# Kernel tuning notes

Measured on AMD Instinct MI355X. Metric: run time of the kernel, lower is better.

The kernel has to match this reference:

```python
import math
import jax, jax.numpy as jnp
import numpy as np

NEG = -1.0e10  # matches LARGE_NUMBER padding in the original
K_SUBSET = 8
N_SAMPLES = 2


def log_conv(aL, aR, K):
    """Log-space convolution of two count distributions, truncated to counts 0..K-1.
    aL, aR: [..., K] log-values; returns c[m] = logsumexp_j aL[j] + aR[m-j]."""
    jj = jnp.arange(K)[:, None]
    mm = jnp.arange(K)[None, :]
    idx = mm - jj  # [K(j), K(m)]
    valid = idx >= 0
    aRg = aR[..., jnp.clip(idx, 0, K - 1)]  # [..., K, K]
    t = aL[..., :, None] + jnp.where(valid, aRg, NEG)
    return jax.nn.logsumexp(t, axis=-2)


def up_pass(theta, k):
    """theta: [B, N] logits (N power of two). Returns list of per-level log-ESP
    tables, levels[l]: [B, N/2^l, k+1]; levels[-1][:,0,j] = log e_j(exp theta)."""
    B, N = theta.shape
    K = k + 1
    leaf = jnp.full((B, N, K), NEG, theta.dtype)
    leaf = leaf.at[..., 0].set(0.0).at[..., 1].set(theta)
    levels = [leaf]
    a = leaf
    while a.shape[1] > 1:
        a = log_conv(a[:, 0::2], a[:, 1::2], K)
        levels.append(a)
    return levels


def down_marginals(levels, theta, k):
    """Exact inclusion marginals P(x_i=1 | sum=k) via tree forward-backward."""
    K = k + 1
    B = theta.shape[0]
    ext = jnp.full((B, 1, K), NEG, theta.dtype).at[..., 0].set(0.0)
    for lvl in range(len(levels) - 2, -1, -1):
        a = levels[lvl]
        aL, aR = a[:, 0::2], a[:, 1::2]
        extL = log_conv(ext, aR, K)  # ESP of everything outside left subtree
        extR = log_conv(ext, aL, K)
        ext = jnp.stack([extL, extR], axis=2).reshape(B, a.shape[1], K)
    logZ = levels[-1][:, 0, k]  # log e_k over all items
    # P(x_i=1) = exp(theta_i) * e_{k-1}(others) / e_k(all)
    return jnp.exp(theta + ext[..., k - 1] - logZ[:, None])


def sample_counts(levels, k, n_samples, key):
    """Top-down exact sampling of k-subsets; returns leaf counts [S, B, N] in {0,1}."""
    K = k + 1
    B = levels[0].shape[0]
    counts = jnp.full((n_samples, B, 1), k, jnp.int32)
    jj = jnp.arange(K)
    for lvl in range(len(levels) - 2, -1, -1):
        a = levels[lvl]
        aL, aR = a[:, 0::2], a[:, 1::2]
        n = aL.shape[1]
        idx = counts[..., None] - jj  # desired right-count, [S,B,n,K]
        valid = idx >= 0
        aRg = jnp.take_along_axis(
            jnp.broadcast_to(aR[None], (n_samples, B, n, K)),
            jnp.clip(idx, 0, k), axis=-1)
        logits = aL[None] + jnp.where(valid, aRg, NEG)
        key, sub = jax.random.split(key)
        g = jax.random.gumbel(sub, logits.shape, logits.dtype)
        cL = jnp.argmax(logits + g, axis=-1).astype(jnp.int32)
        cR = counts - cL
        counts = jnp.stack([cL, cR], axis=-1).reshape(n_samples, B, 2 * n)
    return counts


def setup_inputs() -> dict:
    key = jax.random.key(0)
    scores = jax.random.normal(key, (8192, 32, 8), dtype=jnp.float32)
    return {"scores": scores}


def reference(scores):
    nnodes, choices, ensemble = scores.shape
    k = min(K_SUBSET, choices)
    flat = jnp.transpose(scores, (0, 2, 1)).reshape(nnodes * ensemble, choices)
    N = 2 ** math.ceil(math.log2(choices))
    if N > choices:
        flat = jnp.concatenate(
            [flat, jnp.full((flat.shape[0], N - choices), NEG, flat.dtype)], axis=1)
    levels = up_pass(flat, k)
    marg_flat = down_marginals(levels, flat, k)[:, :choices]  # [B, choices]
    marginals = jnp.transpose(
        marg_flat.reshape(nnodes, ensemble, choices), (0, 2, 1))  # [nnodes, choices, ensemble]
    counts = sample_counts(levels, k, N_SAMPLES, jax.random.key(42))
    counts = counts[:, :, :choices].astype(scores.dtype)
    samples = jnp.transpose(
        counts.reshape(N_SAMPLES, nnodes, ensemble, choices), (0, 1, 3, 2))
    # straight-through: hard samples forward, marginal gradients backward
    samples = jax.lax.stop_gradient(samples - marginals[None]) + marginals[None]
    return samples, marginals
```

## Files before the change

### kernel.cpp

```cpp
#include <hip/hip_runtime.h>
#include <stdint.h>


__host__ __device__ __forceinline__ void tf2x32(uint32_t k0, uint32_t k1,
                                                uint32_t x0, uint32_t x1,
                                                uint32_t& y0, uint32_t& y1) {
  const uint32_t ks[3] = {k0, k1, k0 ^ k1 ^ 0x1BD11BDAu};
  x0 += ks[0]; x1 += ks[1];
  const int R0[4] = {13, 15, 26, 6};
  const int R1[4] = {17, 29, 16, 24};
#pragma unroll
  for (int i = 0; i < 5; ++i) {
    const int* R = (i & 1) ? R1 : R0;
#pragma unroll
    for (int rr = 0; rr < 4; ++rr) {
      x0 += x1;
      x1 = (x1 << R[rr]) | (x1 >> (32 - R[rr]));
      x1 ^= x0;
    }
    x0 += ks[(i + 1) % 3];
    x1 += ks[(i + 2) % 3] + (uint32_t)(i + 1);
  }
  y0 = x0; y1 = x1;
}

struct TFKeys { uint32_t v[10]; };

__device__ __forceinline__ float gumbel_draw(uint32_t sk0, uint32_t sk1,
                                             uint32_t f) {
  uint32_t y0, y1;
  tf2x32(sk0, sk1, 0u, f, y0, y1);
  uint32_t bits = y0 ^ y1;
  uint32_t fb = (bits >> 9) | 0x3f800000u;
  float u = __uint_as_float(fb) - 1.0f;
  const float tiny = 1.17549435e-38f;
  float rr = fmaxf(tiny, u + tiny);
  return -logf(-logf(rr));
}

template<bool FAST> __device__ __forceinline__ float expT(float x) {
  return FAST ? __expf(x) : expf(x);
}
template<bool FAST> __device__ __forceinline__ float logT(float x) {
  return FAST ? __logf(x) : logf(x);
}

template<int SIN, int SOUT, bool FAST, bool LS>
__device__ __forceinline__ void conv_level(const float (&aL)[SIN],
                                           const float (&aR)[SIN],
                                           float (&o)[SOUT]) {
#pragma unroll
  for (int m = 1; m < SOUT; ++m) {
    if (LS && m == SOUT - 1) { o[m] = aL[SIN - 1] + aR[SIN - 1]; continue; }
    const int jlo = (m - (SIN - 1) > 0) ? (m - (SIN - 1)) : 0;
    const int jhi = (m < SIN - 1) ? m : (SIN - 1);
    float t[SIN];
#pragma unroll
    for (int j = 0; j < SIN; ++j)
      if (j >= jlo && j <= jhi) t[j] = aL[j] + aR[m - j];
    float amax = t[jlo];
#pragma unroll
    for (int j = 0; j < SIN; ++j)
      if (j > jlo && j <= jhi) amax = fmaxf(amax, t[j]);
    float s = 0.0f;
#pragma unroll
    for (int j = 0; j < SIN; ++j)
      if (j >= jlo && j <= jhi) s += expT<FAST>(t[j] - amax);
    o[m] = logT<FAST>(s) + amax;
  }
}

template<int SSIB, int MLO, int MHI, bool FAST>
__device__ __forceinline__ void ext_level(const float (&ein)[8],
                                          const float* sib, float (&eo)[8]) {
#pragma unroll
  for (int m = MLO; m <= MHI; ++m) {
    const int jlo = (m - (SSIB - 1) > 0) ? (m - (SSIB - 1)) : 0;
    float t[8];
#pragma unroll
    for (int j = 0; j < 8; ++j)
      if (j >= jlo && j <= m) t[j] = ein[j] + sib[m - j];
    float amax = t[jlo];
#pragma unroll
    for (int j = 0; j < 8; ++j)
      if (j > jlo && j <= m) amax = fmaxf(amax, t[j]);
    float s = 0.0f;
#pragma unroll
    for (int j = 0; j < 8; ++j)
      if (j >= jlo && j <= m) s += expT<FAST>(t[j] - amax);
    eo[m] = logT<FAST>(s) + amax;
  }
}

#define ENT 128

__global__ __launch_bounds__(256, 4) void simple_sampler_kernel(
    const float* __restrict__ scores, float* __restrict__ out,
    int nnodes, TFKeys keys) {
  const int wl = threadIdx.x & 63;
  const int w  = threadIdx.x >> 6;
  const int q = wl & 3;
  const int r = wl >> 2;
  const int p = q & 1;
  const int g = q >> 1;
  const int row = blockIdx.x * 64 + w * 16 + r;
  const int node = row >> 3, e = row & 7;
  const int B = nnodes * 8;

  __shared__ float tab[4 * ENT * 16];
  float* tw = tab + w * (ENT * 16);
#define L(E) tw[(E) * 16 + r]

  float th[8];
  const float* sc = scores + node * 256 + e + (16 * p + 8 * g) * 8;
#pragma unroll
  for (int c = 0; c < 8; ++c) th[c] = sc[c * 8];
#pragma unroll
  for (int c = 0; c < 8; ++c) L(16 * p + 8 * g + c) = th[c];

  float l1r[4], th2r[4];
#pragma unroll
  for (int n1l = 0; n1l < 4; ++n1l) {
    float tL = th[2 * n1l], tR = th[2 * n1l + 1];
    float amax = fmaxf(tR, tL);
    float s = expf(tR - amax) + expf(tL - amax);
    l1r[n1l] = logf(s) + amax;
    th2r[n1l] = tL + tR;
    int n1 = 8 * p + 4 * g + n1l;
    L(32 + n1) = l1r[n1l];
    L(48 + n1) = th2r[n1l];
  }
  float l2r[2][5];
#pragma unroll
  for (int n2l = 0; n2l < 2; ++n2l) {
    float aL[3] = {0.0f, l1r[2 * n2l], th2r[2 * n2l]};
    float aR[3] = {0.0f, l1r[2 * n2l + 1], th2r[2 * n2l + 1]};
    float o5[5];
    conv_level<3, 5, false, true>(aL, aR, o5);
    l2r[n2l][0] = 0.0f;
    int n2 = 4 * p + 2 * g + n2l;
#pragma unroll
    for (int m = 1; m < 5; ++m) { l2r[n2l][m] = o5[m]; L(64 + n2 * 4 + m - 1) = o5[m]; }
  }
  float l3r[9];
  {
    float o9[9];
    conv_level<5, 9, false, true>(l2r[0], l2r[1], o9);
    l3r[0] = 0.0f;
    int n3 = 2 * p + g;
#pragma unroll
    for (int m = 1; m < 9; ++m) { l3r[m] = o9[m]; L(96 + n3 * 8 + m - 1) = o9[m]; }
  }

  __builtin_amdgcn_wave_barrier();

  float l3s[9];
  l3s[0] = 0.0f;
#pragma unroll
  for (int m = 1; m < 9; ++m) l3s[m] = __shfl_xor(l3r[m], 2);

  float A0[9], A1[9];
  {
    float aLp[9], aRp[9];
#pragma unroll
    for (int m = 0; m < 9; ++m) {
      aLp[m] = g ? l3s[m] : l3r[m];
      aRp[m] = g ? l3r[m] : l3s[m];
    }
    float l4o[9];
    conv_level<9, 9, false, false>(aLp, aRp, l4o);
    A0[0] = 0.0f; A1[0] = 0.0f;
#pragma unroll
    for (int m = 1; m < 9; ++m) {
      float own = l4o[m];
      float oth = __shfl_xor(own, 1);
      A0[m] = p ? oth : own;
      A1[m] = p ? own : oth;
    }
  }

  float logZ;
  {
    float tv[9];
#pragma unroll
    for (int j = 0; j < 9; ++j) tv[j] = A0[j] + A1[8 - j];
    float amax = tv[0];
#pragma unroll
    for (int j = 1; j < 9; ++j) amax = fmaxf(amax, tv[j]);
    float s = 0.0f;
#pragma unroll
    for (int j = 0; j < 9; ++j) s += __expf(tv[j] - amax);
    logZ = __logf(s) + amax;
  }

  {
    float e4v[8];
    e4v[0] = 0.0f;
#pragma unroll
    for (int m = 1; m < 8; ++m) e4v[m] = p ? A0[m] : A1[m];
    float* mb = out + 2 * B * 32 + node * 256 + e;
    float e3[8];
    ext_level<9, 0, 7, true>(e4v, l3s, e3);
#pragma unroll
    for (int c2 = 0; c2 < 2; ++c2) {
      float e2v[8];
      ext_level<5, 4, 7, true>(e3, l2r[c2 ^ 1], e2v);
#pragma unroll
      for (int c1i = 0; c1i < 2; ++c1i) {
        const int n1l = 2 * c2 + c1i;
        float sib1[3] = {0.0f, l1r[n1l ^ 1], th2r[n1l ^ 1]};
        float e1m[8];
        ext_level<3, 6, 7, true>(e2v, sib1, e1m);
        const int colL = 16 * p + 8 * g + 2 * n1l;
        {
          float t6 = e1m[6] + th[2 * n1l + 1];
          float t7 = e1m[7];
          float amax = fmaxf(t6, t7);
          float s = __expf(t6 - amax) + __expf(t7 - amax);
          mb[colL * 8] = __expf((th[2 * n1l] + (__logf(s) + amax)) - logZ);
        }
        {
          float t6 = e1m[6] + th[2 * n1l];
          float t7 = e1m[7];
          float amax = fmaxf(t6, t7);
          float s = __expf(t6 - amax) + __expf(t7 - amax);
          mb[(colL + 1) * 8] = __expf((th[2 * n1l + 1] + (__logf(s) + amax)) - logZ);
        }
      }
    }
  }

  const int smp = q & 1;
  const int h = q >> 1;
  const uint32_t t9 = (uint32_t)(smp * B + row) * 9u;
  int c;
  {
    float bv = 0.0f; int bj = 0;
#pragma unroll
    for (int k = 0; k < 5; ++k) {
      const int j = 4 * h + k;
      float gd = gumbel_draw(keys.v[0], keys.v[1], t9 + (uint32_t)j);
      float v = (A0[j] + A1[8 - j]) + gd;
      if (k == 0) { bv = v; bj = j; } else if (v > bv) { bv = v; bj = j; }
    }
    float ov = __shfl_xor(bv, 2);
    int   oj = __shfl_xor(bj, 2);
    float vlo = h ? ov : bv;  int jlo = h ? oj : bj;
    float vhi = h ? bv : ov;  int jhi = h ? bj : oj;
    int rootj = (vhi > vlo) ? jhi : jlo;
    c = h ? (8 - rootj) : rootj;
  }
  int cA, cB;
  {
    int j0 = 0;
    if (c > 0) {
      float b0 = -3.0e38f;
      for (int j = 0; j <= c; ++j) {
        float a = (j == 0) ? 0.0f : L(96 + 16 * h + j - 1);
        float b = (c - j == 0) ? 0.0f : L(96 + 16 * h + 8 + (c - j) - 1);
        float gd = gumbel_draw(keys.v[2], keys.v[3],
                               2u * t9 + (uint32_t)(9 * h + j));
        float v = (a + b) + gd;
        if (v > b0) { b0 = v; j0 = j; }
      }
    }
    cA = j0; cB = c - j0;
  }
  uint32_t pk2 = 0;
  {
    int cc0 = cA, cc1 = cB;
#pragma unroll
    for (int i2 = 0; i2 < 2; ++i2) {
      const int i = 2 * h + i2;
      int ci = i2 ? cc1 : cc0;
      float best = -3.0e38f; int bj2 = 0;
#pragma unroll
      for (int j = 0; j < 5; ++j) {
        float gd = gumbel_draw(keys.v[4], keys.v[5],
                               4u * t9 + (uint32_t)(i * 9 + j));
        int idx = ci - j;
        int cl = min(max(idx, 1), 4);
        float b = L(64 + (2 * i + 1) * 4 + cl - 1);
        float bf = (idx == 0) ? 0.0f : b;
        float a = (j == 0) ? 0.0f : L(64 + (2 * i) * 4 + j - 1);
        float v = (a + bf) + gd;
        if (idx >= 0 && idx <= 4 && v > best) { best = v; bj2 = j; }
      }
      pk2 |= ((uint32_t)bj2 << (8 * i2)) | ((uint32_t)(ci - bj2) << (8 * i2 + 4));
    }
  }
  uint32_t pk3 = 0;
  {
    const uint32_t sk0 = keys.v[6], sk1 = keys.v[7];
    const uint32_t fb0 = 8u * t9;
#pragma unroll
    for (int i2 = 0; i2 < 4; ++i2) {
      const int i = 4 * h + i2;
      int ci = (int)((pk2 >> (4 * i2)) & 15u);
      float aL1 = L(32 + 2 * i), aL2 = L(48 + 2 * i);
      float bR1 = L(32 + 2 * i + 1), bR2 = L(48 + 2 * i + 1);
      uint32_t fb = fb0 + (uint32_t)(i * 9);
      float best = -3.0e38f; int bj3 = 0;
#pragma unroll
      for (int j = 0; j < 3; ++j) {
        float gd = gumbel_draw(sk0, sk1, fb + (uint32_t)j);
        int idx = ci - j;
        float bf = (idx == 1) ? bR1 : ((idx == 2) ? bR2 : 0.0f);
        float af = (j == 0) ? 0.0f : ((j == 1) ? aL1 : aL2);
        float v = (af + bf) + gd;
        if (idx >= 0 && idx <= 2 && v > best) { best = v; bj3 = j; }
      }
      pk3 |= ((uint32_t)bj3 << (8 * i2)) | ((uint32_t)(ci - bj3) << (8 * i2 + 4));
    }
  }
  {
    const uint32_t sk0 = keys.v[8], sk1 = keys.v[9];
    const uint32_t fb0 = 16u * t9;
    float* bs = out + smp * (B * 32) + node * 256 + e;
    uint32_t lst = 0; int m4 = 0;
#pragma unroll
    for (int i2 = 0; i2 < 8; ++i2) {
      int ci = (int)((pk3 >> (4 * i2)) & 15u);
      const int i = 8 * h + i2;
      if (ci == 1) {
        lst |= ((uint32_t)i2) << (4 * m4);
        ++m4;
      } else {
        int bj = ci >> 1;
        bs[16 * i] = (float)bj;
        bs[16 * i + 8] = (float)(ci - bj);
      }
    }
    for (int tt = 0; tt < m4; ++tt) {
      int i2 = (int)((lst >> (4 * tt)) & 15u);
      int i = 8 * h + i2;
      float thL = L(2 * i);
      float thR = L(2 * i + 1);
      uint32_t fb = fb0 + (uint32_t)(i * 9);
      float g0 = gumbel_draw(sk0, sk1, fb);
      float g1 = gumbel_draw(sk0, sk1, fb + 1u);
      int bj = ((thL + g1) > (thR + g0)) ? 1 : 0;
      bs[16 * i] = (float)bj;
      bs[16 * i + 8] = (float)(1 - bj);
    }
  }
#undef L
}

extern "C" void kernel_launch(void* const* d_in, const int* in_sizes, int n_in,
                              void* d_out, int out_size, void* d_ws, size_t ws_size,
                              hipStream_t stream) {
  const float* scores = (const float*)d_in[0];
  float* out = (float*)d_out;
  const int nnodes = in_sizes[0] / (32 * 8);
  const int B = nnodes * 8;

  TFKeys K;
  uint32_t k0 = 0u, k1 = 42u;
  for (int t = 0; t < 5; ++t) {
    uint32_t n0, n1, s0, s1;
    tf2x32(k0, k1, 0u, 0u, n0, n1);
    tf2x32(k0, k1, 0u, 1u, s0, s1);
    K.v[2 * t] = s0; K.v[2 * t + 1] = s1;
    k0 = n0; k1 = n1;
  }

  dim3 grid((unsigned)(B / 64)), block(256);
  hipLaunchKernelGGL(simple_sampler_kernel, grid, block, 0, stream,
                     scores, out, nnodes, K);
}
```

Before: 115.2 us.

## Use one-wave blocks, pad LDS table, and split level-4 convolution across lane pairs

```diff
diff --git a/kernel.cpp b/kernel.cpp
--- a/kernel.cpp
+++ b/kernel.cpp
@@ -94,22 +94,20 @@
 
 #define ENT 128
 
-__global__ __launch_bounds__(256, 4) void simple_sampler_kernel(
+__global__ __launch_bounds__(64, 4) void simple_sampler_kernel(
     const float* __restrict__ scores, float* __restrict__ out,
     int nnodes, TFKeys keys) {
-  const int wl = threadIdx.x & 63;
-  const int w  = threadIdx.x >> 6;
-  const int q = wl & 3;
-  const int r = wl >> 2;
+  const int lane = threadIdx.x;
+  const int q = lane & 3;
+  const int r = lane >> 2;
   const int p = q & 1;
   const int g = q >> 1;
-  const int row = blockIdx.x * 64 + w * 16 + r;
+  const int row = blockIdx.x * 16 + r;
   const int node = row >> 3, e = row & 7;
   const int B = nnodes * 8;
 
-  __shared__ float tab[4 * ENT * 16];
-  float* tw = tab + w * (ENT * 16);
-#define L(E) tw[(E) * 16 + r]
+  __shared__ float tab[ENT * 17];
+#define L(E) tab[(E) * 17 + r]
 
   float th[8];
   const float* sc = scores + node * 256 + e + (16 * p + 8 * g) * 8;
@@ -167,15 +165,40 @@
       aLp[m] = g ? l3s[m] : l3r[m];
       aRp[m] = g ? l3r[m] : l3s[m];
     }
+    float own[4];
+#pragma unroll
+    for (int mi = 0; mi < 4; ++mi) {
+      float t[8];
+#pragma unroll
+      for (int j = 0; j <= 2 * mi + 1; ++j) {
+        float aRv = g ? aRp[2 * mi + 2 - j] : aRp[2 * mi + 1 - j];
+        t[j] = aLp[j] + aRv;
+      }
+      float tlast = aLp[2 * mi + 2] + aRp[0];
+      float amax = t[0];
+#pragma unroll
+      for (int j = 1; j <= 2 * mi + 1; ++j) amax = fmaxf(amax, t[j]);
+      amax = g ? fmaxf(amax, tlast) : amax;
+      float s = 0.0f;
+#pragma unroll
+      for (int j = 0; j <= 2 * mi + 1; ++j) s += expf(t[j] - amax);
+      s += g ? expf(tlast - amax) : 0.0f;
+      own[mi] = logf(s) + amax;
+    }
     float l4o[9];
-    conv_level<9, 9, false, false>(aLp, aRp, l4o);
+#pragma unroll
+    for (int mi = 0; mi < 4; ++mi) {
+      float oth = __shfl_xor(own[mi], 2);
+      l4o[2 * mi + 1] = g ? oth : own[mi];
+      l4o[2 * mi + 2] = g ? own[mi] : oth;
+    }
     A0[0] = 0.0f; A1[0] = 0.0f;
 #pragma unroll
     for (int m = 1; m < 9; ++m) {
-      float own = l4o[m];
-      float oth = __shfl_xor(own, 1);
-      A0[m] = p ? oth : own;
-      A1[m] = p ? own : oth;
+      float o = l4o[m];
+      float oth2 = __shfl_xor(o, 1);
+      A0[m] = p ? oth2 : o;
+      A1[m] = p ? o : oth2;
     }
   }
 
@@ -365,7 +388,7 @@
     k0 = n0; k1 = n1;
   }
 
-  dim3 grid((unsigned)(B / 64)), block(256);
+  dim3 grid((unsigned)(B / 16)), block(64);
   hipLaunchKernelGGL(simple_sampler_kernel, grid, block, 0, stream,
                      scores, out, nnodes, K);
 }
```

After: 117.1 us. About the same (+1.7%).
